# Kernel optimization log

Hardware: AMD Instinct MI355X
Metric: run time of the kernel (lower is better)

The kernel has to match this reference:

```python
import jax, jax.numpy as jnp
import numpy as np

D_MODEL, D_STATE, D_CONV = 768, 8, 3
D_INNER = D_MODEL  # expand = 1
BATCH, SEQ = 4, 8192


def setup_inputs() -> dict:
    key = jax.random.key(0)
    ks = jax.random.split(key, 7)
    x = jax.random.normal(ks[0], (BATCH, SEQ, D_MODEL), dtype=jnp.float32)
    W_in = jax.random.normal(ks[1], (D_MODEL, 2 * D_INNER), dtype=jnp.float32) * 0.02
    conv_w = jax.random.normal(ks[2], (D_INNER, 1, D_CONV), dtype=jnp.float32) * 0.1
    conv_b = jnp.zeros((D_INNER,), dtype=jnp.float32)
    B = jax.random.normal(ks[3], (D_INNER, D_STATE), dtype=jnp.float32)
    C = jax.random.normal(ks[4], (D_INNER, D_STATE), dtype=jnp.float32)
    D = jnp.ones((D_INNER,), dtype=jnp.float32)
    W_out = jax.random.normal(ks[5], (D_INNER, D_MODEL), dtype=jnp.float32) * 0.02
    return {"x": x, "W_in": W_in, "conv_w": conv_w, "conv_b": conv_b,
            "B": B, "C": C, "D": D, "W_out": W_out}


def _forward(x, W_in, conv_w, conv_b, B, C, D, W_out):
    # in_proj and chunk
    xz = x @ W_in                                   # [B, L, 2*d_inner]
    xc, z = jnp.split(xz, 2, axis=-1)               # each [B, L, d_inner]
    # depthwise causal conv1d: torch pads (d_conv-1) both sides then slices [:L]
    # == left-pad (d_conv-1), no right pad
    xc = jnp.transpose(xc, (0, 2, 1))               # [B, d_inner, L]
    xc = jax.lax.conv_general_dilated(
        xc, conv_w,
        window_strides=(1,), padding=[(D_CONV - 1, 0)],
        dimension_numbers=("NCH", "OIH", "NCH"),
        feature_group_count=D_INNER)
    xc = xc + conv_b[None, :, None]
    xc = jnp.transpose(xc, (0, 2, 1))               # [B, L, d_inner]
    xc = jax.nn.silu(xc)
    z = jax.nn.silu(z)
    # simple SSM: h_t = h_{t-1} + outer(u_t, B); y_t = sum_s h_t*C + u_t*D
    # => y = cumsum_t(u) * sum_s(B*C) + u*D   (exact algebraic identity)
    BC = jnp.sum(B * C, axis=-1)                    # [d_inner]
    y = jnp.cumsum(xc, axis=1) * BC + xc * D
    out = (y * z) @ W_out                           # [B, L, d_model]
    return out


def reference(x, W_in, conv_w, conv_b, B, C, D, W_out):
    return _forward(x, W_in, conv_w, conv_b, B, C, D, W_out)
```

## Files before the change

### kernel.cpp

```cpp
#include <hip/hip_runtime.h>
#include <hip/hip_bf16.h>

#define D_MODEL 768
#define NSEQ    8192
#define NBATCH  4
#define MROWS   (NBATCH*NSEQ)
#define CHUNK   128
#define NCHUNK  (NSEQ/CHUNK)

#define BM 128
#define BN 192
#define BK 64

typedef __attribute__((ext_vector_type(8)))  short bshort8;
typedef __attribute__((ext_vector_type(16))) float f32x16;

__device__ __forceinline__ float bf2f(ushort u){
  union { unsigned int i; float f; } x; x.i = ((unsigned int)u) << 16; return x.f;
}
__device__ __forceinline__ ushort f2bf(float f){
  union { float f; unsigned int i; } x; x.f = f;
  unsigned int r = x.i + 0x7fffu + ((x.i >> 16) & 1u);
  return (ushort)(r >> 16);
}
__device__ __forceinline__ float silu_f(float v){ return v / (1.0f + __expf(-v)); }

__device__ __forceinline__ void async_copy16(const ushort* g, ushort* l){
  __builtin_amdgcn_global_load_lds((const __attribute__((address_space(1))) void*)g,
                                   (__attribute__((address_space(3))) void*)l, 16, 0, 0);
}

__global__ void tr_cvt(const float* __restrict__ in, ushort* __restrict__ out, int R, int C){
  __shared__ float tile[32][33];
  int c0 = blockIdx.x*32, r0 = blockIdx.y*32;
  int tx = threadIdx.x & 31, ty = threadIdx.x >> 5;
  #pragma unroll
  for (int p=0;p<4;p++){
    int r = ty + p*8;
    tile[r][tx] = in[(size_t)(r0+r)*C + c0 + tx];
  }
  __syncthreads();
  #pragma unroll
  for (int p=0;p<4;p++){
    int c = ty + p*8;
    out[(size_t)(c0+c)*R + r0 + tx] = f2bf(tile[tx][c]);
  }
}

__global__ void cvt_bf16(const float* __restrict__ in, ushort* __restrict__ out, int n){
  int i = (blockIdx.x*256 + threadIdx.x)*8;
  if (i >= n) return;
  const float4 f0 = *(const float4*)(in + i);
  const float4 f1 = *(const float4*)(in + i + 4);
  ushort o[8];
  o[0]=f2bf(f0.x); o[1]=f2bf(f0.y); o[2]=f2bf(f0.z); o[3]=f2bf(f0.w);
  o[4]=f2bf(f1.x); o[5]=f2bf(f1.y); o[6]=f2bf(f1.z); o[7]=f2bf(f1.w);
  *(ulonglong2*)(out + i) = *(const ulonglong2*)o;
}

__global__ __launch_bounds__(256) void gemm1_bt(
    const ushort* __restrict__ A, const ushort* __restrict__ BT,
    ushort* __restrict__ oxc, ushort* __restrict__ oz, int K)
{
  __shared__ __align__(16) ushort Asm[2][BM*BK];
  __shared__ __align__(16) ushort Bsm[2][BN*BK];
  const int tid = threadIdx.x;
  const int bm = blockIdx.x, bn = blockIdx.y;
  const int lane = tid & 63, wid = tid >> 6;
  const int wm = (wid >> 1) * 64, wn = (wid & 1) * 96;
  const int l31 = lane & 31, half = lane >> 5;

  const ushort* Ag[4]; int aoff[4];
  #pragma unroll
  for (int it=0; it<4; ++it){
    int p  = it*256 + tid;
    int r  = p >> 3;
    int cl = (p & 7) ^ (r & 7);
    Ag[it] = A + (size_t)(bm*BM + r)*K + cl*8;
    aoff[it] = p*8;
  }
  const ushort* Bg[6]; int boff[6];
  #pragma unroll
  for (int it=0; it<6; ++it){
    int p  = it*256 + tid;
    int r  = p >> 3;
    int cl = (p & 7) ^ (r & 7);
    Bg[it] = BT + (size_t)(bn*BN + r)*K + cl*8;
    boff[it] = p*8;
  }

  int arow[2], ar7[2], brow[3], br7[3];
  #pragma unroll
  for (int i=0;i<2;i++){
    int ra = wm + i*32 + l31; arow[i] = ra*BK; ar7[i] = ra & 7;
  }
  #pragma unroll
  for (int j=0;j<3;j++){
    int rb = wn + j*32 + l31; brow[j] = rb*BK; br7[j] = rb & 7;
  }

  f32x16 acc[2][3];
  #pragma unroll
  for (int i=0;i<2;i++)
    #pragma unroll
    for (int j=0;j<3;j++)
      #pragma unroll
      for (int r=0;r<16;r++) acc[i][j][r] = 0.f;

  const int KT = K / BK;

  #pragma unroll
  for (int it=0; it<4; ++it){ async_copy16(Ag[it], &Asm[0][aoff[it]]); Ag[it] += BK; }
  #pragma unroll
  for (int it=0; it<6; ++it){ async_copy16(Bg[it], &Bsm[0][boff[it]]); Bg[it] += BK; }

  int cur = 0;
  for (int kt=0; kt<KT; ++kt){
    __builtin_amdgcn_sched_barrier(0);
    asm volatile("s_waitcnt vmcnt(0)" ::: "memory");
    __builtin_amdgcn_s_barrier();
    __builtin_amdgcn_sched_barrier(0);
    if (kt+1 < KT){
      #pragma unroll
      for (int it=0; it<4; ++it){ async_copy16(Ag[it], &Asm[cur^1][aoff[it]]); Ag[it] += BK; }
      #pragma unroll
      for (int it=0; it<6; ++it){ async_copy16(Bg[it], &Bsm[cur^1][boff[it]]); Bg[it] += BK; }
    }
    const ushort* As = &Asm[cur][0];
    const ushort* Bs = &Bsm[cur][0];
    #pragma unroll
    for (int s=0; s<4; ++s){
      const int c = s*2 + half;
      bshort8 av[2], bv[3];
      #pragma unroll
      for (int i=0;i<2;i++)
        av[i] = *(const bshort8*)(As + arow[i] + ((c ^ ar7[i]) << 3));
      #pragma unroll
      for (int j=0;j<3;j++)
        bv[j] = *(const bshort8*)(Bs + brow[j] + ((c ^ br7[j]) << 3));
      #pragma unroll
      for (int i=0;i<2;i++)
        #pragma unroll
        for (int j=0;j<3;j++)
          acc[i][j] = __builtin_amdgcn_mfma_f32_32x32x16_bf16(av[i], bv[j], acc[i][j], 0,0,0);
    }
    cur ^= 1;
  }

  if (bn < 4){
    #pragma unroll
    for (int i=0;i<2;i++){
      const int Rbase = bm*BM + wm + i*32 + 4*half;
      #pragma unroll
      for (int j=0;j<3;j++){
        const int Cc = bn*BN + wn + j*32 + l31;
        #pragma unroll
        for (int reg=0; reg<16; reg++){
          const int R = Rbase + (reg & 3) + 8*(reg >> 2);
          oxc[(size_t)R*768 + Cc] = f2bf(acc[i][j][reg]);
        }
      }
    }
  } else {
    #pragma unroll
    for (int i=0;i<2;i++){
      const int Rbase = bm*BM + wm + i*32 + 4*half;
      #pragma unroll
      for (int j=0;j<3;j++){
        const int Cc = bn*BN - 768 + wn + j*32 + l31;
        #pragma unroll
        for (int reg=0; reg<16; reg++){
          const int R = Rbase + (reg & 3) + 8*(reg >> 2);
          oz[(size_t)R*768 + Cc] = f2bf(silu_f(acc[i][j][reg]));
        }
      }
    }
  }
}

#define BM2 64
__global__ __launch_bounds__(256) void gemm2_bt(
    const ushort* __restrict__ A, const ushort* __restrict__ BT,
    float* __restrict__ of, int K)
{
  __shared__ __align__(16) ushort Asm[2][BM2*BK];
  __shared__ __align__(16) ushort Bsm[2][BN*BK];
  const int tid = threadIdx.x;
  const int bm = blockIdx.x, bn = blockIdx.y;
  const int lane = tid & 63, wid = tid >> 6;
  const int wm = (wid >> 1) * 32, wn = (wid & 1) * 96;
  const int l31 = lane & 31, half = lane >> 5;

  const ushort* Ag[2]; int aoff[2];
  #pragma unroll
  for (int it=0; it<2; ++it){
    int p  = it*256 + tid;
    int r  = p >> 3;
    int cl = (p & 7) ^ (r & 7);
    Ag[it] = A + (size_t)(bm*BM2 + r)*K + cl*8;
    aoff[it] = p*8;
  }
  const ushort* Bg[6]; int boff[6];
  #pragma unroll
  for (int it=0; it<6; ++it){
    int p  = it*256 + tid;
    int r  = p >> 3;
    int cl = (p & 7) ^ (r & 7);
    Bg[it] = BT + (size_t)(bn*BN + r)*K + cl*8;
    boff[it] = p*8;
  }

  int arow, ar7, brow[3], br7[3];
  { int ra = wm + l31; arow = ra*BK; ar7 = ra & 7; }
  #pragma unroll
  for (int j=0;j<3;j++){
    int rb = wn + j*32 + l31; brow[j] = rb*BK; br7[j] = rb & 7;
  }

  f32x16 acc[3];
  #pragma unroll
  for (int j=0;j<3;j++)
    #pragma unroll
    for (int r=0;r<16;r++) acc[j][r] = 0.f;

  const int KT = K / BK;

  #pragma unroll
  for (int it=0; it<2; ++it){ async_copy16(Ag[it], &Asm[0][aoff[it]]); Ag[it] += BK; }
  #pragma unroll
  for (int it=0; it<6; ++it){ async_copy16(Bg[it], &Bsm[0][boff[it]]); Bg[it] += BK; }

  int cur = 0;
  for (int kt=0; kt<KT; ++kt){
    __builtin_amdgcn_sched_barrier(0);
    asm volatile("s_waitcnt vmcnt(0)" ::: "memory");
    __builtin_amdgcn_s_barrier();
    __builtin_amdgcn_sched_barrier(0);
    if (kt+1 < KT){
      #pragma unroll
      for (int it=0; it<2; ++it){ async_copy16(Ag[it], &Asm[cur^1][aoff[it]]); Ag[it] += BK; }
      #pragma unroll
      for (int it=0; it<6; ++it){ async_copy16(Bg[it], &Bsm[cur^1][boff[it]]); Bg[it] += BK; }
    }
    const ushort* As = &Asm[cur][0];
    const ushort* Bs = &Bsm[cur][0];
    #pragma unroll
    for (int s=0; s<4; ++s){
      const int c = s*2 + half;
      bshort8 av, bv[3];
      av = *(const bshort8*)(As + arow + ((c ^ ar7) << 3));
      #pragma unroll
      for (int j=0;j<3;j++)
        bv[j] = *(const bshort8*)(Bs + brow[j] + ((c ^ br7[j]) << 3));
      #pragma unroll
      for (int j=0;j<3;j++)
        acc[j] = __builtin_amdgcn_mfma_f32_32x32x16_bf16(av, bv[j], acc[j], 0,0,0);
    }
    cur ^= 1;
  }

  const int Rbase = bm*BM2 + wm + 4*half;
  #pragma unroll
  for (int j=0;j<3;j++){
    const int Cc = bn*BN + wn + j*32 + l31;
    #pragma unroll
    for (int reg=0; reg<16; reg++){
      const int R = Rbase + (reg & 3) + 8*(reg >> 2);
      of[(size_t)R*768 + Cc] = acc[j][reg];
    }
  }
}

__global__ void conv_psum(const ushort* __restrict__ xc, const float* __restrict__ cw,
                          const float* __restrict__ cb, float* __restrict__ psum){
  int c0 = threadIdx.x * 2;
  int b = blockIdx.z, ch = blockIdx.x;
  int t0 = ch*CHUNK;
  const ushort* xp = xc + (size_t)b*NSEQ*768 + c0;
  float w0a=cw[c0*3+0], w1a=cw[c0*3+1], w2a=cw[c0*3+2], ba=cb[c0];
  float w0b=cw[c0*3+3], w1b=cw[c0*3+4], w2b=cw[c0*3+5], bb=cb[c0+1];
  float am2=0.f, am1=0.f, bm2=0.f, bm1=0.f;
  if (t0>=2){ ushort2 u = *(const ushort2*)(xp + (size_t)(t0-2)*768); am2=bf2f(u.x); bm2=bf2f(u.y); }
  if (t0>=1){ ushort2 u = *(const ushort2*)(xp + (size_t)(t0-1)*768); am1=bf2f(u.x); bm1=bf2f(u.y); }
  float sa=0.f, sb=0.f;
  #pragma unroll 4
  for (int i=0;i<CHUNK;i++){
    ushort2 u = *(const ushort2*)(xp + (size_t)(t0+i)*768);
    float xa = bf2f(u.x), xb = bf2f(u.y);
    sa += silu_f(w0a*am2 + w1a*am1 + w2a*xa + ba);
    sb += silu_f(w0b*bm2 + w1b*bm1 + w2b*xb + bb);
    am2=am1; am1=xa; bm2=bm1; bm1=xb;
  }
  float2* pp = (float2*)(psum + ((size_t)b*NCHUNK + ch)*768 + c0);
  *pp = make_float2(sa, sb);
}

__global__ void scan_chunks(const float* __restrict__ psum, float* __restrict__ offs){
  int idx = blockIdx.x*256 + threadIdx.x;
  int b = idx/768, c = idx%768;
  float run = 0.f;
  for (int ch=0; ch<NCHUNK; ch++){
    size_t o = ((size_t)b*NCHUNK + ch)*768 + c;
    offs[o] = run;
    run += psum[o];
  }
}

__global__ void scan_apply(const ushort* __restrict__ xc, const ushort* __restrict__ zb,
                           const float* __restrict__ cw, const float* __restrict__ cb,
                           const float* __restrict__ Bm, const float* __restrict__ Cm,
                           const float* __restrict__ Dv, const float* __restrict__ offs,
                           ushort* __restrict__ v){
  int c0 = threadIdx.x * 2;
  int b = blockIdx.z, ch = blockIdx.x;
  int t0 = ch*CHUNK;
  size_t base = (size_t)b*NSEQ*768 + c0;
  const ushort* xp = xc + base;
  const ushort* zp = zb + base;
  ushort* vp = v + base;
  float w0a=cw[c0*3+0], w1a=cw[c0*3+1], w2a=cw[c0*3+2], ba=cb[c0];
  float w0b=cw[c0*3+3], w1b=cw[c0*3+4], w2b=cw[c0*3+5], bb=cb[c0+1];
  float bca=0.f, bcb=0.f;
  #pragma unroll
  for (int s=0;s<8;s++){ bca += Bm[c0*8+s]*Cm[c0*8+s]; bcb += Bm[c0*8+8+s]*Cm[c0*8+8+s]; }
  float dda = Dv[c0], ddb = Dv[c0+1];
  const float2 off2 = *(const float2*)(offs + ((size_t)b*NCHUNK + ch)*768 + c0);
  float cua = off2.x, cub = off2.y;
  float am2=0.f, am1=0.f, bm2=0.f, bm1=0.f;
  if (t0>=2){ ushort2 u = *(const ushort2*)(xp + (size_t)(t0-2)*768); am2=bf2f(u.x); bm2=bf2f(u.y); }
  if (t0>=1){ ushort2 u = *(const ushort2*)(xp + (size_t)(t0-1)*768); am1=bf2f(u.x); bm1=bf2f(u.y); }
  #pragma unroll 4
  for (int i=0;i<CHUNK;i++){
    size_t o = (size_t)(t0+i)*768;
    ushort2 u = *(const ushort2*)(xp + o);
    ushort2 z2 = *(const ushort2*)(zp + o);
    float xa = bf2f(u.x), xb = bf2f(u.y);
    float ua = silu_f(w0a*am2 + w1a*am1 + w2a*xa + ba);
    float ub = silu_f(w0b*bm2 + w1b*bm1 + w2b*xb + bb);
    cua += ua; cub += ub;
    float ya = bca*cua + dda*ua;
    float yb = bcb*cub + ddb*ub;
    ushort2 o2; o2.x = f2bf(ya * bf2f(z2.x)); o2.y = f2bf(yb * bf2f(z2.y));
    *(ushort2*)(vp + o) = o2;
    am2=am1; am1=xa; bm2=bm1; bm1=xb;
  }
}

extern "C" void kernel_launch(void* const* d_in, const int* in_sizes, int n_in,
                              void* d_out, int out_size, void* d_ws, size_t ws_size,
                              hipStream_t stream)
{
  const float* x      = (const float*)d_in[0];
  const float* W_in   = (const float*)d_in[1];
  const float* conv_w = (const float*)d_in[2];
  const float* conv_b = (const float*)d_in[3];
  const float* Bm     = (const float*)d_in[4];
  const float* Cm     = (const float*)d_in[5];
  const float* Dv     = (const float*)d_in[6];
  const float* W_out  = (const float*)d_in[7];
  float* out = (float*)d_out;

  char* ws = (char*)d_ws;
  ushort* xbf   = (ushort*)(ws + 0);
  ushort* xcbf  = (ushort*)(ws + 50331648);
  ushort* zbf   = (ushort*)(ws + 100663296);
  ushort* wint  = (ushort*)(ws + 150994944);
  ushort* woutt = (ushort*)(ws + 153354240);
  float*  psum  = (float*)(ws + 154533888);
  float*  offs  = (float*)(ws + 155320320);
  if (ws_size < 156106752) return;

  tr_cvt<<<dim3(1536/32, 768/32), 256, 0, stream>>>(W_in,  wint,  768, 1536);
  tr_cvt<<<dim3(768/32,  768/32), 256, 0, stream>>>(W_out, woutt, 768, 768);
  cvt_bf16<<<(MROWS*768)/2048, 256, 0, stream>>>(x, xbf, MROWS*768);

  gemm1_bt<<<dim3(MROWS/BM, 1536/BN), 256, 0, stream>>>(xbf, wint, xcbf, zbf, 768);

  conv_psum  <<<dim3(NCHUNK, 1, NBATCH), 384, 0, stream>>>(xcbf, conv_w, conv_b, psum);
  scan_chunks<<<12, 256, 0, stream>>>(psum, offs);
  scan_apply <<<dim3(NCHUNK, 1, NBATCH), 384, 0, stream>>>(xcbf, zbf, conv_w, conv_b,
                                                           Bm, Cm, Dv, offs, xbf );

  gemm2_bt<<<dim3(MROWS/BM2, 768/BN), 256, 0, stream>>>(xbf, woutt, out, 768);
}
```

Baseline: 430.0 us.

## Load GEMM A operands directly to registers with two-stage prefetch, stage only B in LDS

```diff
diff --git a/kernel.cpp b/kernel.cpp
--- a/kernel.cpp
+++ b/kernel.cpp
@@ -58,11 +58,10 @@
   *(ulonglong2*)(out + i) = *(const ulonglong2*)o;
 }
 
-__global__ __launch_bounds__(256) void gemm1_bt(
+__global__ __launch_bounds__(256,2) void gemm1_bt(
     const ushort* __restrict__ A, const ushort* __restrict__ BT,
     ushort* __restrict__ oxc, ushort* __restrict__ oz, int K)
 {
-  __shared__ __align__(16) ushort Asm[2][BM*BK];
   __shared__ __align__(16) ushort Bsm[2][BN*BK];
   const int tid = threadIdx.x;
   const int bm = blockIdx.x, bn = blockIdx.y;
@@ -70,15 +69,6 @@
   const int wm = (wid >> 1) * 64, wn = (wid & 1) * 96;
   const int l31 = lane & 31, half = lane >> 5;
 
-  const ushort* Ag[4]; int aoff[4];
-  #pragma unroll
-  for (int it=0; it<4; ++it){
-    int p  = it*256 + tid;
-    int r  = p >> 3;
-    int cl = (p & 7) ^ (r & 7);
-    Ag[it] = A + (size_t)(bm*BM + r)*K + cl*8;
-    aoff[it] = p*8;
-  }
   const ushort* Bg[6]; int boff[6];
   #pragma unroll
   for (int it=0; it<6; ++it){
@@ -89,11 +79,12 @@
     boff[it] = p*8;
   }
 
-  int arow[2], ar7[2], brow[3], br7[3];
-  #pragma unroll
-  for (int i=0;i<2;i++){
-    int ra = wm + i*32 + l31; arow[i] = ra*BK; ar7[i] = ra & 7;
-  }
+  const ushort* Ap[2];
+  #pragma unroll
+  for (int i=0;i<2;i++)
+    Ap[i] = A + (size_t)(bm*BM + wm + i*32 + l31)*K + half*8;
+
+  int brow[3], br7[3];
   #pragma unroll
   for (int j=0;j<3;j++){
     int rb = wn + j*32 + l31; brow[j] = rb*BK; br7[j] = rb & 7;
@@ -107,45 +98,141 @@
       #pragma unroll
       for (int r=0;r<16;r++) acc[i][j][r] = 0.f;
 
-  const int KT = K / BK;
-
-  #pragma unroll
-  for (int it=0; it<4; ++it){ async_copy16(Ag[it], &Asm[0][aoff[it]]); Ag[it] += BK; }
-  #pragma unroll
-  for (int it=0; it<6; ++it){ async_copy16(Bg[it], &Bsm[0][boff[it]]); Bg[it] += BK; }
-
-  int cur = 0;
-  for (int kt=0; kt<KT; ++kt){
-    __builtin_amdgcn_sched_barrier(0);
-    asm volatile("s_waitcnt vmcnt(0)" ::: "memory");
+  ushort* buf0 = &Bsm[0][0];
+  ushort* buf1 = &Bsm[1][0];
+
+  #pragma unroll
+  for (int it=0; it<6; ++it) async_copy16(Bg[it], buf0 + boff[it]);
+  __builtin_amdgcn_sched_barrier(0);
+  bshort8 a0[2][4], a1[2][4];
+  #pragma unroll
+  for (int i=0;i<2;i++)
+    #pragma unroll
+    for (int s=0;s<4;s++)
+      a0[i][s] = *(const bshort8*)(Ap[i] + 0*64 + s*16);
+  __builtin_amdgcn_sched_barrier(0);
+  #pragma unroll
+  for (int i=0;i<2;i++)
+    #pragma unroll
+    for (int s=0;s<4;s++)
+      a1[i][s] = *(const bshort8*)(Ap[i] + 1*64 + s*16);
+  __builtin_amdgcn_sched_barrier(0);
+
+  for (int kt=0; kt<10; kt+=2){
+    asm volatile("s_waitcnt vmcnt(8)" ::: "memory");
+    __builtin_amdgcn_sched_barrier(0);
     __builtin_amdgcn_s_barrier();
     __builtin_amdgcn_sched_barrier(0);
-    if (kt+1 < KT){
-      #pragma unroll
-      for (int it=0; it<4; ++it){ async_copy16(Ag[it], &Asm[cur^1][aoff[it]]); Ag[it] += BK; }
-      #pragma unroll
-      for (int it=0; it<6; ++it){ async_copy16(Bg[it], &Bsm[cur^1][boff[it]]); Bg[it] += BK; }
-    }
-    const ushort* As = &Asm[cur][0];
-    const ushort* Bs = &Bsm[cur][0];
-    #pragma unroll
-    for (int s=0; s<4; ++s){
-      const int c = s*2 + half;
-      bshort8 av[2], bv[3];
+    #pragma unroll
+    for (int it=0; it<6; ++it) async_copy16(Bg[it] + (kt+1)*BK, buf1 + boff[it]);
+    __builtin_amdgcn_sched_barrier(0);
+    {
+      bshort8 n[2][4];
       #pragma unroll
       for (int i=0;i<2;i++)
-        av[i] = *(const bshort8*)(As + arow[i] + ((c ^ ar7[i]) << 3));
+        #pragma unroll
+        for (int s=0;s<4;s++)
+          n[i][s] = *(const bshort8*)(Ap[i] + (kt+2)*64 + s*16);
+      __builtin_amdgcn_sched_barrier(0);
+      __builtin_amdgcn_s_setprio(1);
+      #pragma unroll
+      for (int s=0; s<4; ++s){
+        const int c = s*2 + half;
+        bshort8 bv[3];
+        #pragma unroll
+        for (int j=0;j<3;j++)
+          bv[j] = *(const bshort8*)(buf0 + brow[j] + ((c ^ br7[j]) << 3));
+        #pragma unroll
+        for (int i=0;i<2;i++)
+          #pragma unroll
+          for (int j=0;j<3;j++)
+            acc[i][j] = __builtin_amdgcn_mfma_f32_32x32x16_bf16(a0[i][s], bv[j], acc[i][j], 0,0,0);
+      }
+      __builtin_amdgcn_s_setprio(0);
+      #pragma unroll
+      for (int i=0;i<2;i++)
+        #pragma unroll
+        for (int s=0;s<4;s++)
+          a0[i][s] = n[i][s];
+    }
+    asm volatile("s_waitcnt vmcnt(8)" ::: "memory");
+    __builtin_amdgcn_sched_barrier(0);
+    __builtin_amdgcn_s_barrier();
+    __builtin_amdgcn_sched_barrier(0);
+    #pragma unroll
+    for (int it=0; it<6; ++it) async_copy16(Bg[it] + (kt+2)*BK, buf0 + boff[it]);
+    __builtin_amdgcn_sched_barrier(0);
+    {
+      bshort8 n[2][4];
+      #pragma unroll
+      for (int i=0;i<2;i++)
+        #pragma unroll
+        for (int s=0;s<4;s++)
+          n[i][s] = *(const bshort8*)(Ap[i] + (kt+3)*64 + s*16);
+      __builtin_amdgcn_sched_barrier(0);
+      __builtin_amdgcn_s_setprio(1);
+      #pragma unroll
+      for (int s=0; s<4; ++s){
+        const int c = s*2 + half;
+        bshort8 bv[3];
+        #pragma unroll
+        for (int j=0;j<3;j++)
+          bv[j] = *(const bshort8*)(buf1 + brow[j] + ((c ^ br7[j]) << 3));
+        #pragma unroll
+        for (int i=0;i<2;i++)
+          #pragma unroll
+          for (int j=0;j<3;j++)
+            acc[i][j] = __builtin_amdgcn_mfma_f32_32x32x16_bf16(a1[i][s], bv[j], acc[i][j], 0,0,0);
+      }
+      __builtin_amdgcn_s_setprio(0);
+      #pragma unroll
+      for (int i=0;i<2;i++)
+        #pragma unroll
+        for (int s=0;s<4;s++)
+          a1[i][s] = n[i][s];
+    }
+  }
+  asm volatile("s_waitcnt vmcnt(8)" ::: "memory");
+  __builtin_amdgcn_sched_barrier(0);
+  __builtin_amdgcn_s_barrier();
+  __builtin_amdgcn_sched_barrier(0);
+  #pragma unroll
+  for (int it=0; it<6; ++it) async_copy16(Bg[it] + 11*BK, buf1 + boff[it]);
+  __builtin_amdgcn_sched_barrier(0);
+  __builtin_amdgcn_s_setprio(1);
+  #pragma unroll
+  for (int s=0; s<4; ++s){
+    const int c = s*2 + half;
+    bshort8 bv[3];
+    #pragma unroll
+    for (int j=0;j<3;j++)
+      bv[j] = *(const bshort8*)(buf0 + brow[j] + ((c ^ br7[j]) << 3));
+    #pragma unroll
+    for (int i=0;i<2;i++)
       #pragma unroll
       for (int j=0;j<3;j++)
-        bv[j] = *(const bshort8*)(Bs + brow[j] + ((c ^ br7[j]) << 3));
-      #pragma unroll
-      for (int i=0;i<2;i++)
-        #pragma unroll
-        for (int j=0;j<3;j++)
-          acc[i][j] = __builtin_amdgcn_mfma_f32_32x32x16_bf16(av[i], bv[j], acc[i][j], 0,0,0);
-    }
-    cur ^= 1;
-  }
+        acc[i][j] = __builtin_amdgcn_mfma_f32_32x32x16_bf16(a0[i][s], bv[j], acc[i][j], 0,0,0);
+  }
+  __builtin_amdgcn_s_setprio(0);
+  asm volatile("s_waitcnt vmcnt(0)" ::: "memory");
+  __builtin_amdgcn_sched_barrier(0);
+  __builtin_amdgcn_s_barrier();
+  __builtin_amdgcn_sched_barrier(0);
+  __builtin_amdgcn_s_setprio(1);
+  #pragma unroll
+  for (int s=0; s<4; ++s){
+    const int c = s*2 + half;
+    bshort8 bv[3];
+    #pragma unroll
+    for (int j=0;j<3;j++)
+      bv[j] = *(const bshort8*)(buf1 + brow[j] + ((c ^ br7[j]) << 3));
+    #pragma unroll
+    for (int i=0;i<2;i++)
+      #pragma unroll
+      for (int j=0;j<3;j++)
+        acc[i][j] = __builtin_amdgcn_mfma_f32_32x32x16_bf16(a1[i][s], bv[j], acc[i][j], 0,0,0);
+  }
+  __builtin_amdgcn_s_setprio(0);
 
   if (bn < 4){
     #pragma unroll
@@ -179,11 +266,10 @@
 }
 
 #define BM2 64
-__global__ __launch_bounds__(256) void gemm2_bt(
+__global__ __launch_bounds__(256,2) void gemm2_bt(
     const ushort* __restrict__ A, const ushort* __restrict__ BT,
     float* __restrict__ of, int K)
 {
-  __shared__ __align__(16) ushort Asm[2][BM2*BK];
   __shared__ __align__(16) ushort Bsm[2][BN*BK];
   const int tid = threadIdx.x;
   const int bm = blockIdx.x, bn = blockIdx.y;
@@ -191,15 +277,6 @@
   const int wm = (wid >> 1) * 32, wn = (wid & 1) * 96;
   const int l31 = lane & 31, half = lane >> 5;
 
-  const ushort* Ag[2]; int aoff[2];
-  #pragma unroll
-  for (int it=0; it<2; ++it){
-    int p  = it*256 + tid;
-    int r  = p >> 3;
-    int cl = (p & 7) ^ (r & 7);
-    Ag[it] = A + (size_t)(bm*BM2 + r)*K + cl*8;
-    aoff[it] = p*8;
-  }
   const ushort* Bg[6]; int boff[6];
   #pragma unroll
   for (int it=0; it<6; ++it){
@@ -210,8 +287,9 @@
     boff[it] = p*8;
   }
 
-  int arow, ar7, brow[3], br7[3];
-  { int ra = wm + l31; arow = ra*BK; ar7 = ra & 7; }
+  const ushort* Ap = A + (size_t)(bm*BM2 + wm + l31)*K + half*8;
+
+  int brow[3], br7[3];
   #pragma unroll
   for (int j=0;j<3;j++){
     int rb = wn + j*32 + l31; brow[j] = rb*BK; br7[j] = rb & 7;
@@ -223,41 +301,115 @@
     #pragma unroll
     for (int r=0;r<16;r++) acc[j][r] = 0.f;
 
-  const int KT = K / BK;
-
-  #pragma unroll
-  for (int it=0; it<2; ++it){ async_copy16(Ag[it], &Asm[0][aoff[it]]); Ag[it] += BK; }
-  #pragma unroll
-  for (int it=0; it<6; ++it){ async_copy16(Bg[it], &Bsm[0][boff[it]]); Bg[it] += BK; }
-
-  int cur = 0;
-  for (int kt=0; kt<KT; ++kt){
-    __builtin_amdgcn_sched_barrier(0);
-    asm volatile("s_waitcnt vmcnt(0)" ::: "memory");
+  ushort* buf0 = &Bsm[0][0];
+  ushort* buf1 = &Bsm[1][0];
+
+  #pragma unroll
+  for (int it=0; it<6; ++it) async_copy16(Bg[it], buf0 + boff[it]);
+  __builtin_amdgcn_sched_barrier(0);
+  bshort8 a0[4], a1[4];
+  #pragma unroll
+  for (int s=0;s<4;s++) a0[s] = *(const bshort8*)(Ap + 0*64 + s*16);
+  __builtin_amdgcn_sched_barrier(0);
+  #pragma unroll
+  for (int s=0;s<4;s++) a1[s] = *(const bshort8*)(Ap + 1*64 + s*16);
+  __builtin_amdgcn_sched_barrier(0);
+
+  for (int kt=0; kt<10; kt+=2){
+    asm volatile("s_waitcnt vmcnt(4)" ::: "memory");
+    __builtin_amdgcn_sched_barrier(0);
     __builtin_amdgcn_s_barrier();
     __builtin_amdgcn_sched_barrier(0);
-    if (kt+1 < KT){
-      #pragma unroll
-      for (int it=0; it<2; ++it){ async_copy16(Ag[it], &Asm[cur^1][aoff[it]]); Ag[it] += BK; }
-      #pragma unroll
-      for (int it=0; it<6; ++it){ async_copy16(Bg[it], &Bsm[cur^1][boff[it]]); Bg[it] += BK; }
-    }
-    const ushort* As = &Asm[cur][0];
-    const ushort* Bs = &Bsm[cur][0];
-    #pragma unroll
-    for (int s=0; s<4; ++s){
-      const int c = s*2 + half;
-      bshort8 av, bv[3];
-      av = *(const bshort8*)(As + arow + ((c ^ ar7) << 3));
-      #pragma unroll
-      for (int j=0;j<3;j++)
-        bv[j] = *(const bshort8*)(Bs + brow[j] + ((c ^ br7[j]) << 3));
-      #pragma unroll
-      for (int j=0;j<3;j++)
-        acc[j] = __builtin_amdgcn_mfma_f32_32x32x16_bf16(av, bv[j], acc[j], 0,0,0);
-    }
-    cur ^= 1;
-  }
+    #pragma unroll
+    for (int it=0; it<6; ++it) async_copy16(Bg[it] + (kt+1)*BK, buf1 + boff[it]);
+    __builtin_amdgcn_sched_barrier(0);
+    {
+      bshort8 n[4];
+      #pragma unroll
+      for (int s=0;s<4;s++) n[s] = *(const bshort8*)(Ap + (kt+2)*64 + s*16);
+      __builtin_amdgcn_sched_barrier(0);
+      __builtin_amdgcn_s_setprio(1);
+      #pragma unroll
+      for (int s=0; s<4; ++s){
+        const int c = s*2 + half;
+        bshort8 bv[3];
+        #pragma unroll
+        for (int j=0;j<3;j++)
+          bv[j] = *(const bshort8*)(buf0 + brow[j] + ((c ^ br7[j]) << 3));
+        #pragma unroll
+        for (int j=0;j<3;j++)
+          acc[j] = __builtin_amdgcn_mfma_f32_32x32x16_bf16(a0[s], bv[j], acc[j], 0,0,0);
+      }
+      __builtin_amdgcn_s_setprio(0);
+      #pragma unroll
+      for (int s=0;s<4;s++) a0[s] = n[s];
+    }
+    asm volatile("s_waitcnt vmcnt(4)" ::: "memory");
+    __builtin_amdgcn_sched_barrier(0);
+    __builtin_amdgcn_s_barrier();
+    __builtin_amdgcn_sched_barrier(0);
+    #pragma unroll
+    for (int it=0; it<6; ++it) async_copy16(Bg[it] + (kt+2)*BK, buf0 + boff[it]);
+    __builtin_amdgcn_sched_barrier(0);
+    {
+      bshort8 n[4];
+      #pragma unroll
+      for (int s=0;s<4;s++) n[s] = *(const bshort8*)(Ap + (kt+3)*64 + s*16);
+      __builtin_amdgcn_sched_barrier(0);
+      __builtin_amdgcn_s_setprio(1);
+      #pragma unroll
+      for (int s=0; s<4; ++s){
+        const int c = s*2 + half;
+        bshort8 bv[3];
+        #pragma unroll
+        for (int j=0;j<3;j++)
+          bv[j] = *(const bshort8*)(buf1 + brow[j] + ((c ^ br7[j]) << 3));
+        #pragma unroll
+        for (int j=0;j<3;j++)
+          acc[j] = __builtin_amdgcn_mfma_f32_32x32x16_bf16(a1[s], bv[j], acc[j], 0,0,0);
+      }
+      __builtin_amdgcn_s_setprio(0);
+      #pragma unroll
+      for (int s=0;s<4;s++) a1[s] = n[s];
+    }
+  }
+  asm volatile("s_waitcnt vmcnt(4)" ::: "memory");
+  __builtin_amdgcn_sched_barrier(0);
+  __builtin_amdgcn_s_barrier();
+  __builtin_amdgcn_sched_barrier(0);
+  #pragma unroll
+  for (int it=0; it<6; ++it) async_copy16(Bg[it] + 11*BK, buf1 + boff[it]);
+  __builtin_amdgcn_sched_barrier(0);
+  __builtin_amdgcn_s_setprio(1);
+  #pragma unroll
+  for (int s=0; s<4; ++s){
+    const int c = s*2 + half;
+    bshort8 bv[3];
+    #pragma unroll
+    for (int j=0;j<3;j++)
+      bv[j] = *(const bshort8*)(buf0 + brow[j] + ((c ^ br7[j]) << 3));
+    #pragma unroll
+    for (int j=0;j<3;j++)
+      acc[j] = __builtin_amdgcn_mfma_f32_32x32x16_bf16(a0[s], bv[j], acc[j], 0,0,0);
+  }
+  __builtin_amdgcn_s_setprio(0);
+  asm volatile("s_waitcnt vmcnt(0)" ::: "memory");
+  __builtin_amdgcn_sched_barrier(0);
+  __builtin_amdgcn_s_barrier();
+  __builtin_amdgcn_sched_barrier(0);
+  __builtin_amdgcn_s_setprio(1);
+  #pragma unroll
+  for (int s=0; s<4; ++s){
+    const int c = s*2 + half;
+    bshort8 bv[3];
+    #pragma unroll
+    for (int j=0;j<3;j++)
+      bv[j] = *(const bshort8*)(buf1 + brow[j] + ((c ^ br7[j]) << 3));
+    #pragma unroll
+    for (int j=0;j<3;j++)
+      acc[j] = __builtin_amdgcn_mfma_f32_32x32x16_bf16(a1[s], bv[j], acc[j], 0,0,0);
+  }
+  __builtin_amdgcn_s_setprio(0);
 
   const int Rbase = bm*BM2 + wm + 4*half;
   #pragma unroll
```

New measurement: 467.4 us. 1.09x slower.
